# Kernel tuning notes

Hardware: AMD Instinct MI355X
Metric: run time of the kernel (lower is better)

Reference implementation:

```python
import jax, jax.numpy as jnp
import numpy as np

HIDDEN = 2048
N_EXPERTS = 8
N_LAYERS = 1
GATING_DIM = 64
TOP_K = 2
BALANCING_COEF = 0.01
NOISE_STD = 0.01
B = 4096


def setup_inputs() -> dict:
    key = jax.random.key(0)
    ks = jax.random.split(key, 12)
    s = 0.02
    return {
        "x": jax.random.normal(ks[0], (B, HIDDEN), jnp.float32),
        "noise": jax.random.normal(ks[1], (B, N_EXPERTS), jnp.float32),
        "gate_w1": jax.random.normal(ks[2], (HIDDEN, GATING_DIM), jnp.float32) * s,
        "gate_b1": jnp.zeros((GATING_DIM,), jnp.float32),
        "gate_w2": jax.random.normal(ks[3], (GATING_DIM, N_EXPERTS), jnp.float32) * s,
        "gate_b2": jnp.zeros((N_EXPERTS,), jnp.float32),
        "shared_w": jax.random.normal(ks[4], (HIDDEN, HIDDEN), jnp.float32) * s,
        "shared_b": jnp.zeros((HIDDEN,), jnp.float32),
        "shared_scale": jnp.float32(1.0),
        "expert_w": jax.random.normal(ks[5], (N_EXPERTS, N_LAYERS, HIDDEN, HIDDEN), jnp.float32) * s,
        "expert_b": jnp.zeros((N_EXPERTS, N_LAYERS, HIDDEN), jnp.float32),
        "router_scale": jnp.float32(1.0),
    }


def reference(x, noise, gate_w1, gate_b1, gate_w2, gate_b2,
              shared_w, shared_b, shared_scale, expert_w, expert_b, router_scale):
    Bn = x.shape[0]
    # gating network: softmax(Linear(ReLU(Linear(x)))) + noise
    h = jax.nn.relu(x @ gate_w1 + gate_b1)
    gating = jax.nn.softmax(h @ gate_w2 + gate_b2, axis=-1) + noise * NOISE_STD  # [B,E]

    topk_w, topk_idx = jax.lax.top_k(gating, TOP_K)  # [B,K]
    topk_w = topk_w / jnp.sum(topk_w, axis=-1, keepdims=True)

    # dense combine weights [B,E] (zero for unrouted experts)
    comb = jnp.zeros((Bn, N_EXPERTS), x.dtype)
    comb = comb.at[jnp.arange(Bn)[:, None], topk_idx].add(topk_w)

    # all experts on all tokens (same math as masked dispatch) -> [E,B,D]
    eh = jnp.broadcast_to(x[None], (N_EXPERTS, Bn, HIDDEN))
    for l in range(N_LAYERS):
        eh = jax.nn.sigmoid(jnp.einsum('ebd,edf->ebf', eh, expert_w[:, l]) + expert_b[:, l][:, None, :]) + eh
    routed = jnp.einsum('ebd,be->bd', eh, comb)

    shared = jax.nn.sigmoid(x @ shared_w + shared_b)
    final_out = x + shared_scale * shared + router_scale * routed

    experts_prob = jnp.mean(gating, axis=0)
    target_prob = jnp.ones((N_EXPERTS,), x.dtype) / N_EXPERTS
    gate_loss = jnp.mean((target_prob - experts_prob) ** 2) * BALANCING_COEF
    return final_out, gate_loss
```

## Files before the change

### kernel.cpp

```cpp
#include <hip/hip_runtime.h>
#include <cstdint>
#include <cstddef>

#define HIDDEN 2048
#define NEXP 8
#define GDIM 64
#define BTOK 4096
#define NOISE_STD 0.01f

#define BM 128
#define BN 128
#define BK 32
#define NT_K (HIDDEN / BK)
#define GTOK 8

typedef unsigned short ushort_t;
typedef short bf16x8 __attribute__((ext_vector_type(8)));
typedef float f32x4 __attribute__((ext_vector_type(4)));
typedef unsigned short ushortx8 __attribute__((ext_vector_type(8)));

__device__ __forceinline__ float sigmoid_fast(float v) {
    return 1.0f / (1.0f + __expf(-v));
}

__device__ __forceinline__ ushort_t f2bf(float f) {
    union { float f; uint32_t u; } v; v.f = f;
    uint32_t r = v.u + 0x7fffu + ((v.u >> 16) & 1u);
    return (ushort_t)(r >> 16);
}

__device__ __forceinline__ void gl2lds16(const ushort_t* g, ushort_t* l) {
    __builtin_amdgcn_global_load_lds(
        (const __attribute__((address_space(1))) unsigned int*)g,
        (__attribute__((address_space(3))) unsigned int*)l, 16, 0, 0);
}

__global__ __launch_bounds__(256) void convert_x_kernel(
    const float* __restrict__ in, ushort_t* __restrict__ out)
{
    const size_t i = ((size_t)blockIdx.x * 256 + threadIdx.x) * 8;
    float4 a = *(const float4*)(in + i);
    float4 b = *(const float4*)(in + i + 4);
    ushortx8 o;
    o[0] = f2bf(a.x); o[1] = f2bf(a.y); o[2] = f2bf(a.z); o[3] = f2bf(a.w);
    o[4] = f2bf(b.x); o[5] = f2bf(b.y); o[6] = f2bf(b.z); o[7] = f2bf(b.w);
    *(ushortx8*)(out + i) = o;
}

__global__ __launch_bounds__(256) void transpose_convert_kernel(
    const float* __restrict__ in, ushort_t* __restrict__ out)
{
    __shared__ float t[64][65];
    const size_t moff = (size_t)blockIdx.z * HIDDEN * HIDDEN;
    const int r0 = blockIdx.y * 64, c0 = blockIdx.x * 64;
    const int tid = threadIdx.x;
    const int tr = tid >> 4, tc = (tid & 15) * 4;
    #pragma unroll
    for (int ii = 0; ii < 4; ++ii) {
        float4 v = *(const float4*)(in + moff + (size_t)(r0 + tr + ii * 16) * HIDDEN + c0 + tc);
        t[tr + ii * 16][tc + 0] = v.x; t[tr + ii * 16][tc + 1] = v.y;
        t[tr + ii * 16][tc + 2] = v.z; t[tr + ii * 16][tc + 3] = v.w;
    }
    __syncthreads();
    const int orow = tid >> 3;
    const int ok = (tid & 7) * 8;
    #pragma unroll
    for (int jj = 0; jj < 2; ++jj) {
        const int c = orow + jj * 32;
        ushortx8 o;
        #pragma unroll
        for (int e = 0; e < 8; ++e) o[e] = f2bf(t[ok + e][c]);
        *(ushortx8*)(out + moff + (size_t)(c0 + c) * HIDDEN + r0 + ok) = o;
    }
}

__global__ __launch_bounds__(256) void gating_kernel(
    const float* __restrict__ x, const float* __restrict__ noise,
    const float* __restrict__ gw1, const float* __restrict__ gb1,
    const float* __restrict__ gw2, const float* __restrict__ gb2,
    float* __restrict__ gating_out, float* __restrict__ wlist,
    int* __restrict__ tlist, int* __restrict__ counts)
{
    const int tid = threadIdx.x;
    const int t0 = blockIdx.x * GTOK;

    __shared__ float xs[GTOK][64];
    __shared__ float hs[GTOK][GDIM + 1];
    __shared__ float logit_s[GTOK][NEXP];

    const int tok = tid >> 5;
    const int jj = (tid & 31) * 2;
    float accx = 0.f, accy = 0.f;

    for (int kc = 0; kc < HIDDEN / 64; ++kc) {
        const int k0 = kc * 64;
        __syncthreads();
        if (tid < 128) {
            const int r = tid >> 4, c4 = (tid & 15) * 4;
            *(float4*)&xs[r][c4] = *(const float4*)(x + (size_t)(t0 + r) * HIDDEN + k0 + c4);
        }
        __syncthreads();
        #pragma unroll 8
        for (int kk = 0; kk < 64; ++kk) {
            const float xv = xs[tok][kk];
            const float2 g = *(const float2*)(gw1 + (size_t)(k0 + kk) * GDIM + jj);
            accx = fmaf(xv, g.x, accx);
            accy = fmaf(xv, g.y, accy);
        }
    }
    hs[tok][jj]     = fmaxf(accx + gb1[jj], 0.f);
    hs[tok][jj + 1] = fmaxf(accy + gb1[jj + 1], 0.f);
    __syncthreads();

    if (tid < GTOK * NEXP) {
        const int t = tid >> 3, e = tid & 7;
        float l = gb2[e];
        #pragma unroll
        for (int j2 = 0; j2 < GDIM; ++j2)
            l = fmaf(hs[t][j2], gw2[j2 * NEXP + e], l);
        logit_s[t][e] = l;
    }
    __syncthreads();

    if (tid < GTOK) {
        const int token = t0 + tid;
        float g[NEXP];
        float m = logit_s[tid][0];
        #pragma unroll
        for (int e = 1; e < NEXP; ++e) m = fmaxf(m, logit_s[tid][e]);
        float se = 0.f;
        #pragma unroll
        for (int e = 0; e < NEXP; ++e) { g[e] = expf(logit_s[tid][e] - m); se += g[e]; }
        float inv = 1.0f / se;
        #pragma unroll
        for (int e = 0; e < NEXP; ++e) {
            g[e] = g[e] * inv + noise[(size_t)token * NEXP + e] * NOISE_STD;
            gating_out[(size_t)token * NEXP + e] = g[e];
        }
        int i1 = 0;
        #pragma unroll
        for (int e = 1; e < NEXP; ++e) if (g[e] > g[i1]) i1 = e;
        int i2 = (i1 == 0) ? 1 : 0;
        #pragma unroll
        for (int e = 0; e < NEXP; ++e) if (e != i1 && g[e] > g[i2]) i2 = e;
        float wsum = g[i1] + g[i2];
        int p1 = atomicAdd(&counts[i1], 1);
        tlist[i1 * BTOK + p1] = token; wlist[i1 * BTOK + p1] = g[i1] / wsum;
        int p2 = atomicAdd(&counts[i2], 1);
        tlist[i2 * BTOK + p2] = token; wlist[i2 * BTOK + p2] = g[i2] / wsum;
    }
}

__global__ __launch_bounds__(256) void loss_kernel(
    const float* __restrict__ gating, float* __restrict__ out_loss)
{
    __shared__ float red[256][NEXP];
    const int tid = threadIdx.x;
    float loc[NEXP];
    #pragma unroll
    for (int e = 0; e < NEXP; ++e) loc[e] = 0.f;
    for (int t = tid; t < BTOK; t += 256) {
        #pragma unroll
        for (int e = 0; e < NEXP; ++e) loc[e] += gating[(size_t)t * NEXP + e];
    }
    #pragma unroll
    for (int e = 0; e < NEXP; ++e) red[tid][e] = loc[e];
    __syncthreads();
    for (int s = 128; s > 0; s >>= 1) {
        if (tid < s) {
            #pragma unroll
            for (int e = 0; e < NEXP; ++e) red[tid][e] += red[tid + s][e];
        }
        __syncthreads();
    }
    if (tid == 0) {
        float loss = 0.f;
        #pragma unroll
        for (int e = 0; e < NEXP; ++e) {
            float p = red[0][e] / (float)BTOK;
            float d = 0.125f - p;
            loss += d * d;
        }
        out_loss[0] = (loss / 8.0f) * 0.01f;
    }
}

__global__ __launch_bounds__(256) void expert_kernel(
    const ushort_t* __restrict__ xb, const ushort_t* __restrict__ ewT,
    const float* __restrict__ eb, const int* __restrict__ counts,
    const int* __restrict__ tlist, const float* __restrict__ wlist,
    float* __restrict__ routed)
{
    const int e = blockIdx.z;
    const int cnt = counts[e];
    const int m0 = blockIdx.y * BM;
    if (m0 >= cnt) return;
    const int n0 = blockIdx.x * BN;
    const ushort_t* __restrict__ wT = ewT + (size_t)e * HIDDEN * HIDDEN;

    __shared__ int rows_s[BM];
    __shared__ float wts_s[BM];
    __shared__ ushort_t sA[2][BM * BK];
    __shared__ ushort_t sB[2][BN * BK];

    const int tid = threadIdx.x;
    if (tid < BM) {
        int mi = m0 + tid;
        if (mi < cnt) { rows_s[tid] = tlist[e * BTOK + mi]; wts_s[tid] = wlist[e * BTOK + mi]; }
        else { rows_s[tid] = -1; wts_s[tid] = 0.f; }
    }
    __syncthreads();

    const int lane = tid & 63;
    const int wid = tid >> 6;
    const int wr = (wid >> 1) * 64;
    const int wc = (wid & 1) * 64;
    const int lr = lane & 15;
    const int sg = (lane >> 4) ^ ((lane >> 1) & 3);

    const int crow = wid * 32 + (lane >> 2);
    const int kgr = (((lane & 3) ^ ((lane >> 3) & 3)) << 3);
    const int tokA0 = max(rows_s[crow], 0);
    const int tokA1 = max(rows_s[crow + 16], 0);
    const ushort_t* srcA0 = xb + (size_t)tokA0 * HIDDEN + kgr;
    const ushort_t* srcA1 = xb + (size_t)tokA1 * HIDDEN + kgr;
    const ushort_t* srcB0 = wT + (size_t)(n0 + crow) * HIDDEN + kgr;
    const ushort_t* srcB1 = wT + (size_t)(n0 + crow + 16) * HIDDEN + kgr;

    f32x4 acc[4][4];
    #pragma unroll
    for (int m = 0; m < 4; ++m)
        #pragma unroll
        for (int n = 0; n < 4; ++n) acc[m][n] = (f32x4){0.f, 0.f, 0.f, 0.f};

    gl2lds16(srcA0, &sA[0][(wid * 32) * BK]);
    gl2lds16(srcA1, &sA[0][(wid * 32 + 16) * BK]);
    gl2lds16(srcB0, &sB[0][(wid * 32) * BK]);
    gl2lds16(srcB1, &sB[0][(wid * 32 + 16) * BK]);
    __syncthreads();

    int cur = 0;
    for (int kt = 0; kt < NT_K; ++kt) {
        if (kt + 1 < NT_K) {
            const int k0 = (kt + 1) * BK;
            gl2lds16(srcA0 + k0, &sA[cur ^ 1][(wid * 32) * BK]);
            gl2lds16(srcA1 + k0, &sA[cur ^ 1][(wid * 32 + 16) * BK]);
            gl2lds16(srcB0 + k0, &sB[cur ^ 1][(wid * 32) * BK]);
            gl2lds16(srcB1 + k0, &sB[cur ^ 1][(wid * 32 + 16) * BK]);
        }
        const ushort_t* Ab = sA[cur];
        const ushort_t* Bb = sB[cur];
        bf16x8 af[4], bfr[4];
        #pragma unroll
        for (int m = 0; m < 4; ++m)
            af[m] = *(const bf16x8*)&Ab[(wr + m * 16 + lr) * BK + sg * 8];
        #pragma unroll
        for (int n = 0; n < 4; ++n)
            bfr[n] = *(const bf16x8*)&Bb[(wc + n * 16 + lr) * BK + sg * 8];
        #pragma unroll
        for (int m = 0; m < 4; ++m)
            #pragma unroll
            for (int n = 0; n < 4; ++n)
                acc[m][n] = __builtin_amdgcn_mfma_f32_16x16x32_bf16(af[m], bfr[n], acc[m][n], 0, 0, 0);
        __syncthreads();
        cur ^= 1;
    }

    float bvn[4];
    #pragma unroll
    for (int n = 0; n < 4; ++n)
        bvn[n] = eb[(size_t)e * HIDDEN + n0 + wc + n * 16 + lr];
    #pragma unroll
    for (int m = 0; m < 4; ++m) {
        #pragma unroll
        for (int q = 0; q < 4; ++q) {
            const int lrow = wr + m * 16 + (lane >> 4) * 4 + q;
            const int r = rows_s[lrow];
            if (r < 0) continue;
            const float wt = wts_s[lrow];
            float* dst = routed + (size_t)r * HIDDEN + n0 + wc + lr;
            #pragma unroll
            for (int n = 0; n < 4; ++n)
                atomicAdd(dst + n * 16, wt * sigmoid_fast(acc[m][n][q] + bvn[n]));
        }
    }
}

__global__ __launch_bounds__(256) void shared_final_kernel(
    const ushort_t* __restrict__ xb, const ushort_t* __restrict__ swT,
    const float* __restrict__ x, const float* __restrict__ bias,
    const float* __restrict__ sscale, const float* __restrict__ rscale,
    const float* __restrict__ routed, float* __restrict__ out)
{
    const int m0 = blockIdx.y * BM;
    const int n0 = blockIdx.x * BN;

    __shared__ ushort_t sA[2][BM * BK];
    __shared__ ushort_t sB[2][BN * BK];

    const int tid = threadIdx.x;
    const int lane = tid & 63;
    const int wid = tid >> 6;
    const int wr = (wid >> 1) * 64;
    const int wc = (wid & 1) * 64;
    const int lr = lane & 15;
    const int sg = (lane >> 4) ^ ((lane >> 1) & 3);

    const int crow = wid * 32 + (lane >> 2);
    const int kgr = (((lane & 3) ^ ((lane >> 3) & 3)) << 3);
    const ushort_t* srcA0 = xb + (size_t)(m0 + crow) * HIDDEN + kgr;
    const ushort_t* srcA1 = xb + (size_t)(m0 + crow + 16) * HIDDEN + kgr;
    const ushort_t* srcB0 = swT + (size_t)(n0 + crow) * HIDDEN + kgr;
    const ushort_t* srcB1 = swT + (size_t)(n0 + crow + 16) * HIDDEN + kgr;

    f32x4 acc[4][4];
    #pragma unroll
    for (int m = 0; m < 4; ++m)
        #pragma unroll
        for (int n = 0; n < 4; ++n) acc[m][n] = (f32x4){0.f, 0.f, 0.f, 0.f};

    gl2lds16(srcA0, &sA[0][(wid * 32) * BK]);
    gl2lds16(srcA1, &sA[0][(wid * 32 + 16) * BK]);
    gl2lds16(srcB0, &sB[0][(wid * 32) * BK]);
    gl2lds16(srcB1, &sB[0][(wid * 32 + 16) * BK]);
    __syncthreads();

    int cur = 0;
    for (int kt = 0; kt < NT_K; ++kt) {
        if (kt + 1 < NT_K) {
            const int k0 = (kt + 1) * BK;
            gl2lds16(srcA0 + k0, &sA[cur ^ 1][(wid * 32) * BK]);
            gl2lds16(srcA1 + k0, &sA[cur ^ 1][(wid * 32 + 16) * BK]);
            gl2lds16(srcB0 + k0, &sB[cur ^ 1][(wid * 32) * BK]);
            gl2lds16(srcB1 + k0, &sB[cur ^ 1][(wid * 32 + 16) * BK]);
        }
        const ushort_t* Ab = sA[cur];
        const ushort_t* Bb = sB[cur];
        bf16x8 af[4], bfr[4];
        #pragma unroll
        for (int m = 0; m < 4; ++m)
            af[m] = *(const bf16x8*)&Ab[(wr + m * 16 + lr) * BK + sg * 8];
        #pragma unroll
        for (int n = 0; n < 4; ++n)
            bfr[n] = *(const bf16x8*)&Bb[(wc + n * 16 + lr) * BK + sg * 8];
        #pragma unroll
        for (int m = 0; m < 4; ++m)
            #pragma unroll
            for (int n = 0; n < 4; ++n)
                acc[m][n] = __builtin_amdgcn_mfma_f32_16x16x32_bf16(af[m], bfr[n], acc[m][n], 0, 0, 0);
        __syncthreads();
        cur ^= 1;
    }

    const float ss = *sscale;
    const float rs = *rscale;
    float bvn[4];
    #pragma unroll
    for (int n = 0; n < 4; ++n)
        bvn[n] = bias[n0 + wc + n * 16 + lr];
    #pragma unroll
    for (int m = 0; m < 4; ++m) {
        #pragma unroll
        for (int q = 0; q < 4; ++q) {
            const int row = m0 + wr + m * 16 + (lane >> 4) * 4 + q;
            const size_t base = (size_t)row * HIDDEN + n0 + wc + lr;
            #pragma unroll
            for (int n = 0; n < 4; ++n) {
                const float xv = x[base + n * 16];
                const float rv = routed[base + n * 16];
                out[base + n * 16] = xv + ss * sigmoid_fast(acc[m][n][q] + bvn[n]) + rs * (xv + rv);
            }
        }
    }
}

extern "C" void kernel_launch(void* const* d_in, const int* in_sizes, int n_in,
                              void* d_out, int out_size, void* d_ws, size_t ws_size,
                              hipStream_t stream) {
    const float* x      = (const float*)d_in[0];
    const float* noise  = (const float*)d_in[1];
    const float* gw1    = (const float*)d_in[2];
    const float* gb1    = (const float*)d_in[3];
    const float* gw2    = (const float*)d_in[4];
    const float* gb2    = (const float*)d_in[5];
    const float* sw     = (const float*)d_in[6];
    const float* sb     = (const float*)d_in[7];
    const float* sscale = (const float*)d_in[8];
    const float* ew     = (const float*)d_in[9];
    const float* ebias  = (const float*)d_in[10];
    const float* rscale = (const float*)d_in[11];
    float* out = (float*)d_out;

    float* ws = (float*)d_ws;
    float* routed   = ws;
    int*   counts   = (int*)(ws + (size_t)BTOK * HIDDEN);
    float* gating   = ws + (size_t)BTOK * HIDDEN + 8;
    int*   tlist    = (int*)(gating + (size_t)BTOK * NEXP);
    float* wlist    = (float*)(tlist + (size_t)NEXP * BTOK);
    ushort_t* xb    = (ushort_t*)(wlist + (size_t)NEXP * BTOK);
    ushort_t* ewT   = xb + (size_t)BTOK * HIDDEN;
    ushort_t* swT   = ewT + (size_t)NEXP * HIDDEN * HIDDEN;

    hipMemsetAsync(d_ws, 0, ((size_t)BTOK * HIDDEN + 8) * sizeof(float), stream);

    convert_x_kernel<<<(BTOK * HIDDEN) / (256 * 8), 256, 0, stream>>>(x, xb);
    transpose_convert_kernel<<<dim3(HIDDEN / 64, HIDDEN / 64, NEXP), 256, 0, stream>>>(ew, ewT);
    transpose_convert_kernel<<<dim3(HIDDEN / 64, HIDDEN / 64, 1), 256, 0, stream>>>(sw, swT);

    gating_kernel<<<BTOK / GTOK, 256, 0, stream>>>(x, noise, gw1, gb1, gw2, gb2,
                                                   gating, wlist, tlist, counts);
    loss_kernel<<<1, 256, 0, stream>>>(gating, out + (size_t)BTOK * HIDDEN);

    expert_kernel<<<dim3(HIDDEN / BN, BTOK / BM, NEXP), 256, 0, stream>>>(
        xb, ewT, ebias, counts, tlist, wlist, routed);
    shared_final_kernel<<<dim3(HIDDEN / BN, BTOK / BM), 256, 0, stream>>>(
        xb, swT, x, sb, sscale, rscale, routed, out);
}
```

Before: 727.4 us.

## Replace atomic scatter of expert outputs with compact bf16 buffer and gather in final kernel

Expert outputs are no longer scattered into a zeroed fp32 routed buffer with atomicAdd. They are written as bf16 into a compacted per-expert-slot buffer, using prefix offsets computed in the loss kernel. The final shared kernel gathers each token's two expert rows through new per-token index and weight arrays and combines them there. This removes the large memset and the fp32 atomic traffic, and workgroup ids are remapped (XCD-style swizzle) for locality; the cost is bf16 rounding of expert outputs and gathered reads in the epilogue.

```diff
diff --git a/kernel.cpp b/kernel.cpp
--- a/kernel.cpp
+++ b/kernel.cpp
@@ -27,6 +27,11 @@
     union { float f; uint32_t u; } v; v.f = f;
     uint32_t r = v.u + 0x7fffu + ((v.u >> 16) & 1u);
     return (ushort_t)(r >> 16);
+}
+
+__device__ __forceinline__ float bf2f(ushort_t u) {
+    union { uint32_t u; float f; } v; v.u = (uint32_t)u << 16;
+    return v.f;
 }
 
 __device__ __forceinline__ void gl2lds16(const ushort_t* g, ushort_t* l) {
@@ -78,8 +83,9 @@
     const float* __restrict__ x, const float* __restrict__ noise,
     const float* __restrict__ gw1, const float* __restrict__ gb1,
     const float* __restrict__ gw2, const float* __restrict__ gb2,
-    float* __restrict__ gating_out, float* __restrict__ wlist,
-    int* __restrict__ tlist, int* __restrict__ counts)
+    float* __restrict__ gating_out, int* __restrict__ tlist,
+    int* __restrict__ counts, int4* __restrict__ tok2i,
+    float2* __restrict__ tok2w)
 {
     const int tid = threadIdx.x;
     const int t0 = blockIdx.x * GTOK;
@@ -145,14 +151,17 @@
         for (int e = 0; e < NEXP; ++e) if (e != i1 && g[e] > g[i2]) i2 = e;
         float wsum = g[i1] + g[i2];
         int p1 = atomicAdd(&counts[i1], 1);
-        tlist[i1 * BTOK + p1] = token; wlist[i1 * BTOK + p1] = g[i1] / wsum;
+        tlist[i1 * BTOK + p1] = token;
         int p2 = atomicAdd(&counts[i2], 1);
-        tlist[i2 * BTOK + p2] = token; wlist[i2 * BTOK + p2] = g[i2] / wsum;
+        tlist[i2 * BTOK + p2] = token;
+        tok2i[token] = make_int4(i1, p1, i2, p2);
+        tok2w[token] = make_float2(g[i1] / wsum, g[i2] / wsum);
     }
 }
 
 __global__ __launch_bounds__(256) void loss_kernel(
-    const float* __restrict__ gating, float* __restrict__ out_loss)
+    const float* __restrict__ gating, const int* __restrict__ counts,
+    int* __restrict__ offs, float* __restrict__ out_loss)
 {
     __shared__ float red[256][NEXP];
     const int tid = threadIdx.x;
@@ -182,32 +191,38 @@
             loss += d * d;
         }
         out_loss[0] = (loss / 8.0f) * 0.01f;
+        int o = 0;
+        #pragma unroll
+        for (int e = 0; e < NEXP; ++e) { offs[e] = o; o += counts[e]; }
+        offs[NEXP] = o;
     }
 }
 
 __global__ __launch_bounds__(256) void expert_kernel(
     const ushort_t* __restrict__ xb, const ushort_t* __restrict__ ewT,
     const float* __restrict__ eb, const int* __restrict__ counts,
-    const int* __restrict__ tlist, const float* __restrict__ wlist,
-    float* __restrict__ routed)
-{
-    const int e = blockIdx.z;
+    const int* __restrict__ offs, const int* __restrict__ tlist,
+    ushort_t* __restrict__ eout)
+{
+    const int orig = blockIdx.x;
+    const int wgid = (orig & 7) * 512 + (orig >> 3);
+    const int e = wgid >> 9;
+    const int rem = wgid & 511;
+    const int n0 = (rem >> 5) * BN;
+    const int m0 = (rem & 31) * BM;
+
     const int cnt = counts[e];
-    const int m0 = blockIdx.y * BM;
     if (m0 >= cnt) return;
-    const int n0 = blockIdx.x * BN;
     const ushort_t* __restrict__ wT = ewT + (size_t)e * HIDDEN * HIDDEN;
 
     __shared__ int rows_s[BM];
-    __shared__ float wts_s[BM];
     __shared__ ushort_t sA[2][BM * BK];
     __shared__ ushort_t sB[2][BN * BK];
 
     const int tid = threadIdx.x;
     if (tid < BM) {
         int mi = m0 + tid;
-        if (mi < cnt) { rows_s[tid] = tlist[e * BTOK + mi]; wts_s[tid] = wlist[e * BTOK + mi]; }
-        else { rows_s[tid] = -1; wts_s[tid] = 0.f; }
+        rows_s[tid] = (mi < cnt) ? tlist[e * BTOK + mi] : -1;
     }
     __syncthreads();
 
@@ -266,6 +281,7 @@
         cur ^= 1;
     }
 
+    const int grow0 = offs[e] + m0;
     float bvn[4];
     #pragma unroll
     for (int n = 0; n < 4; ++n)
@@ -275,13 +291,11 @@
         #pragma unroll
         for (int q = 0; q < 4; ++q) {
             const int lrow = wr + m * 16 + (lane >> 4) * 4 + q;
-            const int r = rows_s[lrow];
-            if (r < 0) continue;
-            const float wt = wts_s[lrow];
-            float* dst = routed + (size_t)r * HIDDEN + n0 + wc + lr;
+            if (rows_s[lrow] < 0) continue;
+            ushort_t* dst = eout + (size_t)(grow0 + lrow) * HIDDEN + n0 + wc + lr;
             #pragma unroll
             for (int n = 0; n < 4; ++n)
-                atomicAdd(dst + n * 16, wt * sigmoid_fast(acc[m][n][q] + bvn[n]));
+                dst[n * 16] = f2bf(sigmoid_fast(acc[m][n][q] + bvn[n]));
         }
     }
 }
@@ -290,10 +304,14 @@
     const ushort_t* __restrict__ xb, const ushort_t* __restrict__ swT,
     const float* __restrict__ x, const float* __restrict__ bias,
     const float* __restrict__ sscale, const float* __restrict__ rscale,
-    const float* __restrict__ routed, float* __restrict__ out)
-{
-    const int m0 = blockIdx.y * BM;
-    const int n0 = blockIdx.x * BN;
+    const ushort_t* __restrict__ eout, const int4* __restrict__ tok2i,
+    const float2* __restrict__ tok2w, const int* __restrict__ offs,
+    float* __restrict__ out)
+{
+    const int orig = blockIdx.x;
+    const int wgid = (orig & 7) * 64 + (orig >> 3);
+    const int n0 = (wgid >> 5) * BN;
+    const int m0 = (wgid & 31) * BM;
 
     __shared__ ushort_t sA[2][BM * BK];
     __shared__ ushort_t sB[2][BN * BK];
@@ -358,16 +376,21 @@
     #pragma unroll
     for (int n = 0; n < 4; ++n)
         bvn[n] = bias[n0 + wc + n * 16 + lr];
+    const int cb = n0 + wc + lr;
     #pragma unroll
     for (int m = 0; m < 4; ++m) {
         #pragma unroll
         for (int q = 0; q < 4; ++q) {
             const int row = m0 + wr + m * 16 + (lane >> 4) * 4 + q;
-            const size_t base = (size_t)row * HIDDEN + n0 + wc + lr;
+            const int4 t2 = tok2i[row];
+            const float2 tw = tok2w[row];
+            const size_t g1 = (size_t)(offs[t2.x] + t2.y) * HIDDEN + cb;
+            const size_t g2 = (size_t)(offs[t2.z] + t2.w) * HIDDEN + cb;
+            const size_t base = (size_t)row * HIDDEN + cb;
             #pragma unroll
             for (int n = 0; n < 4; ++n) {
                 const float xv = x[base + n * 16];
-                const float rv = routed[base + n * 16];
+                const float rv = tw.x * bf2f(eout[g1 + n * 16]) + tw.y * bf2f(eout[g2 + n * 16]);
                 out[base + n * 16] = xv + ss * sigmoid_fast(acc[m][n][q] + bvn[n]) + rs * (xv + rv);
             }
         }
@@ -391,28 +414,31 @@
     const float* rscale = (const float*)d_in[11];
     float* out = (float*)d_out;
 
-    float* ws = (float*)d_ws;
-    float* routed   = ws;
-    int*   counts   = (int*)(ws + (size_t)BTOK * HIDDEN);
-    float* gating   = ws + (size_t)BTOK * HIDDEN + 8;
-    int*   tlist    = (int*)(gating + (size_t)BTOK * NEXP);
-    float* wlist    = (float*)(tlist + (size_t)NEXP * BTOK);
-    ushort_t* xb    = (ushort_t*)(wlist + (size_t)NEXP * BTOK);
-    ushort_t* ewT   = xb + (size_t)BTOK * HIDDEN;
-    ushort_t* swT   = ewT + (size_t)NEXP * HIDDEN * HIDDEN;
-
-    hipMemsetAsync(d_ws, 0, ((size_t)BTOK * HIDDEN + 8) * sizeof(float), stream);
+    char* wsb = (char*)d_ws;
+    ushort_t* eout  = (ushort_t*)wsb;
+    char* p = wsb + (size_t)2 * BTOK * HIDDEN * sizeof(ushort_t);
+    int* counts = (int*)p;            p += 32;
+    int* offs   = (int*)p;            p += 64;
+    float* gating = (float*)p;        p += (size_t)BTOK * NEXP * 4;
+    int* tlist  = (int*)p;            p += (size_t)NEXP * BTOK * 4;
+    int4* tok2i = (int4*)p;           p += (size_t)BTOK * 16;
+    float2* tok2w = (float2*)p;       p += (size_t)BTOK * 8;
+    ushort_t* xb  = (ushort_t*)p;     p += (size_t)BTOK * HIDDEN * 2;
+    ushort_t* ewT = (ushort_t*)p;     p += (size_t)NEXP * HIDDEN * HIDDEN * 2;
+    ushort_t* swT = (ushort_t*)p;
+
+    hipMemsetAsync(counts, 0, 32, stream);
 
     convert_x_kernel<<<(BTOK * HIDDEN) / (256 * 8), 256, 0, stream>>>(x, xb);
     transpose_convert_kernel<<<dim3(HIDDEN / 64, HIDDEN / 64, NEXP), 256, 0, stream>>>(ew, ewT);
     transpose_convert_kernel<<<dim3(HIDDEN / 64, HIDDEN / 64, 1), 256, 0, stream>>>(sw, swT);
 
     gating_kernel<<<BTOK / GTOK, 256, 0, stream>>>(x, noise, gw1, gb1, gw2, gb2,
-                                                   gating, wlist, tlist, counts);
-    loss_kernel<<<1, 256, 0, stream>>>(gating, out + (size_t)BTOK * HIDDEN);
-
-    expert_kernel<<<dim3(HIDDEN / BN, BTOK / BM, NEXP), 256, 0, stream>>>(
-        xb, ewT, ebias, counts, tlist, wlist, routed);
-    shared_final_kernel<<<dim3(HIDDEN / BN, BTOK / BM), 256, 0, stream>>>(
-        xb, swT, x, sb, sscale, rscale, routed, out);
-}
+                                                   gating, tlist, counts, tok2i, tok2w);
+    loss_kernel<<<1, 256, 0, stream>>>(gating, counts, offs, out + (size_t)BTOK * HIDDEN);
+
+    expert_kernel<<<16 * 32 * NEXP, 256, 0, stream>>>(
+        xb, ewT, ebias, counts, offs, tlist, eout);
+    shared_final_kernel<<<16 * 32, 256, 0, stream>>>(
+        xb, swT, x, sb, sscale, rscale, eout, tok2i, tok2w, offs, out);
+}
```

Result: slower. 749.0 us (+3.0%).
